# Kernel optimization log

Hardware: AMD Instinct MI355X
Metric: run time of the kernel (lower is better)

The kernel has to match this reference:

```python
import jax, jax.numpy as jnp
import numpy as np
from jax import lax

H = 128

def _lstm_gates(x, h, c, w_ih, w_hh, b_ih, b_hh):
    # PyTorch gate order: i, f, g, o
    g = x @ w_ih.T + h @ w_hh.T + b_ih + b_hh
    i, f, gg, o = jnp.split(g, 4, axis=-1)
    c_new = jax.nn.sigmoid(f) * c + jax.nn.sigmoid(i) * jnp.tanh(gg)
    h_new = jax.nn.sigmoid(o) * jnp.tanh(c_new)
    return h_new, c_new

def _lstm_layer(x_btF, w_ih, w_hh, b_ih, b_hh):
    B = x_btF.shape[0]
    h0 = jnp.zeros((B, H), x_btF.dtype)
    c0 = jnp.zeros((B, H), x_btF.dtype)
    def step(carry, xt):
        h, c = carry
        h, c = _lstm_gates(xt, h, c, w_ih, w_hh, b_ih, b_hh)
        return (h, c), h
    (h_T, c_T), ys = lax.scan(step, (h0, c0), jnp.swapaxes(x_btF, 0, 1))
    return jnp.swapaxes(ys, 0, 1), h_T, c_T

def setup_inputs() -> dict:
    key = jax.random.key(0)
    ks = jax.random.split(key, 20)
    B, T, D, P = 4096, 200, 2, 3
    s = 1.0 / np.sqrt(H)
    u = lambda k, shp: jax.random.uniform(k, shp, jnp.float32, -s, s)
    return {
        'x_hist': jax.random.normal(ks[0], (B, T, D), jnp.float32),
        'params': jax.random.normal(ks[1], (B, P), jnp.float32),
        'pred_len': 200,
        'w_ih0': u(ks[2], (4 * H, D)), 'w_hh0': u(ks[3], (4 * H, H)),
        'b_ih0': u(ks[4], (4 * H,)), 'b_hh0': u(ks[5], (4 * H,)),
        'w_ih1': u(ks[6], (4 * H, H)), 'w_hh1': u(ks[7], (4 * H, H)),
        'b_ih1': u(ks[8], (4 * H,)), 'b_hh1': u(ks[9], (4 * H,)),
        'dec_w_ih': u(ks[10], (4 * H, D + P)), 'dec_w_hh': u(ks[11], (4 * H, H)),
        'dec_b_ih': u(ks[12], (4 * H,)), 'dec_b_hh': u(ks[13], (4 * H,)),
        'proj_w': u(ks[14], (H, P)), 'proj_b': u(ks[15], (H,)),
        'out_w': u(ks[16], (2, H)), 'out_b': u(ks[17], (2,)),
    }

def reference(x_hist, params, pred_len, w_ih0, w_hh0, b_ih0, b_hh0,
              w_ih1, w_hh1, b_ih1, b_hh1, dec_w_ih, dec_w_hh, dec_b_ih,
              dec_b_hh, proj_w, proj_b, out_w, out_b):
    # 2-layer encoder LSTM; only last layer's final (h, c) are used
    y1, _, _ = _lstm_layer(x_hist, w_ih0, w_hh0, b_ih0, b_hh0)
    _, h_n, c_n = _lstm_layer(y1, w_ih1, w_hh1, b_ih1, b_hh1)
    h = h_n + params @ proj_w.T + proj_b
    c = c_n
    cur = x_hist[:, -1, :]
    def step(carry, _):
        h, c, cur = carry
        inp = jnp.concatenate([cur, params], axis=-1)
        h, c = _lstm_gates(inp, h, c, dec_w_ih, dec_w_hh, dec_b_ih, dec_b_hh)
        cur = h @ out_w.T + out_b
        return (h, c, cur), cur
    _, preds = lax.scan(step, (h, c, cur), None, length=pred_len)
    return jnp.swapaxes(preds, 0, 1)  # [B, pred_len, 2]
```

## Files before the change

kernel.cpp:

```cpp
#include <hip/hip_runtime.h>
#include <stdint.h>

typedef __bf16 bf16x8 __attribute__((ext_vector_type(8)));
typedef float  f32x4  __attribute__((ext_vector_type(4)));

#define PRED   200
#define TSTEPS 200
#define NBLK   256
#define ASTR   280
#define ALO    136
#define ABUFB  (16*ASTR*2)
#define W_BYTES 131072
#define A_OFF   W_BYTES
#define LDS_A   (A_OFF + 2*ABUFB)
#define STG_OFF (A_OFF + 2*ABUFB)
#define LDS_C   (STG_OFF + ABUFB)
#define CP_OFF  (A_OFF + 2*ABUFB)
#define CUR_OFF (CP_OFF + 1024)
#define LDS_D   (CUR_OFF + 128)

#define STATE_FLOATS ((size_t)NBLK*4*2048)

__device__ __forceinline__ float sigm(float x){ return 1.0f/(1.0f+__expf(-x)); }
__device__ __forceinline__ float tanhx(float x){
  float t=__expf(-2.0f*fabsf(x)); float y=(1.0f-t)/(1.0f+t); return copysignf(y,x);
}
__device__ __forceinline__ bf16x8 hi8(float4 a, float4 b){
  bf16x8 r; r[0]=(__bf16)a.x; r[1]=(__bf16)a.y; r[2]=(__bf16)a.z; r[3]=(__bf16)a.w;
  r[4]=(__bf16)b.x; r[5]=(__bf16)b.y; r[6]=(__bf16)b.z; r[7]=(__bf16)b.w; return r;
}
__device__ __forceinline__ bf16x8 lo8(float4 a, float4 b, bf16x8 h){
  bf16x8 r;
  r[0]=(__bf16)(a.x-(float)h[0]); r[1]=(__bf16)(a.y-(float)h[1]);
  r[2]=(__bf16)(a.z-(float)h[2]); r[3]=(__bf16)(a.w-(float)h[3]);
  r[4]=(__bf16)(b.x-(float)h[4]); r[5]=(__bf16)(b.y-(float)h[5]);
  r[6]=(__bf16)(b.z-(float)h[6]); r[7]=(__bf16)(b.w-(float)h[7]); return r;
}
#define MFMA(A,B,C) __builtin_amdgcn_mfma_f32_16x16x32_bf16((A),(B),(C),0,0,0)

__global__ void __launch_bounds__(512,2)
k_l0(const float* __restrict__ xh, const float* __restrict__ wih0,
     const float* __restrict__ whh0, const float* __restrict__ bih0,
     const float* __restrict__ bhh0, float* __restrict__ wsf,
     int chunkStart, int chunkLen, unsigned long long stageFloats)
{
  extern __shared__ char smem[];
  const int tid=threadIdx.x, wv=tid>>6, l=tid&63, c=l&15, qd=l>>4;
  const int hc=wv*16+c, blk=blockIdx.x, r0=blk*16;
  float* stf = wsf + stageFloats;
  #pragma unroll
  for (int i=0;i<16;++i){
    int f=i*8+wv, ntg=f>>2, kt=f&3;
    int g=(ntg&3)*128+(ntg>>2)*16+c, k=kt*32+qd*8;
    const float* s=whh0+g*128+k;
    *(bf16x8*)(smem+f*1024+l*16)=hi8(*(const float4*)s,*(const float4*)(s+4));
  }
  bf16x8 wlo[16];
  #pragma unroll
  for (int tt=0;tt<4;++tt)
    #pragma unroll
    for (int kt=0;kt<4;++kt){
      const float* s=whh0+(size_t)(tt*128+hc)*128+kt*32+qd*8;
      float4 a=*(const float4*)s, b=*(const float4*)(s+4);
      wlo[tt*4+kt]=lo8(a,b,hi8(a,b));
    }
  float b0[4], w0x[4], w0y[4];
  #pragma unroll
  for (int tt=0;tt<4;++tt){
    int g=tt*128+hc;
    b0[tt]=bih0[g]+bhh0[g]; w0x[tt]=wih0[2*g]; w0y[tt]=wih0[2*g+1];
  }
  float c0[4];
  {
    __bf16* B1=(__bf16*)(smem+A_OFF+ABUFB);
    const float* hst=stf+(size_t)(blk*4+0)*2048;
    const float* cst=stf+(size_t)(blk*4+1)*2048;
    #pragma unroll
    for (int i=0;i<4;++i){
      int e=tid*4+i, row=e>>7, col=e&127;
      float v=0.f; if(chunkStart) v=hst[e];
      __bf16 h=(__bf16)v;
      B1[row*ASTR+col]=h; B1[row*ASTR+ALO+col]=(__bf16)(v-(float)h);
    }
    #pragma unroll
    for (int j=0;j<4;++j){ float v=0.f; if(chunkStart) v=cst[(qd*4+j)*128+hc]; c0[j]=v; }
  }
  __syncthreads();
  for (int t=0;t<chunkLen;++t){
    const int p=t&1, tg=chunkStart+t;
    float2 xv[4];
    #pragma unroll
    for (int j=0;j<4;++j) xv[j]=*(const float2*)(xh+(size_t)(r0+qd*4+j)*400+tg*2);
    f32x4 acc[4];
    #pragma unroll
    for (int tt=0;tt<4;++tt) acc[tt]=(f32x4){b0[tt],b0[tt],b0[tt],b0[tt]};
    const char* Ar=smem+A_OFF+(size_t)(1-p)*ABUFB;
    #pragma unroll
    for (int kt=0;kt<4;++kt){
      bf16x8 ah=*(const bf16x8*)(Ar+(c*ASTR+kt*32+qd*8)*2);
      bf16x8 al=*(const bf16x8*)(Ar+(c*ASTR+ALO+kt*32+qd*8)*2);
      #pragma unroll
      for (int tt=0;tt<4;++tt){
        bf16x8 bh=*(const bf16x8*)(smem+(size_t)((wv*4+tt)*4+kt)*1024+l*16);
        acc[tt]=MFMA(ah,bh,acc[tt]);
        acc[tt]=MFMA(al,bh,acc[tt]);
        acc[tt]=MFMA(ah,wlo[tt*4+kt],acc[tt]);
      }
    }
    __bf16* Aw=(__bf16*)(smem+A_OFF+(size_t)p*ABUFB);
    float* h0o=wsf+((size_t)t*NBLK+blk)*2048;
    #pragma unroll
    for (int j=0;j<4;++j){
      float gi=acc[0][j]+xv[j].x*w0x[0]+xv[j].y*w0y[0];
      float gf=acc[1][j]+xv[j].x*w0x[1]+xv[j].y*w0y[1];
      float gg=acc[2][j]+xv[j].x*w0x[2]+xv[j].y*w0y[2];
      float go=acc[3][j]+xv[j].x*w0x[3]+xv[j].y*w0y[3];
      float cn=sigm(gf)*c0[j]+sigm(gi)*tanhx(gg); c0[j]=cn;
      float hn=sigm(go)*tanhx(cn);
      int row=qd*4+j;
      __bf16 hh=(__bf16)hn;
      Aw[row*ASTR+hc]=hh; Aw[row*ASTR+ALO+hc]=(__bf16)(hn-(float)hh);
      h0o[row*128+hc]=hn;
      if (t==chunkLen-1){
        stf[(size_t)(blk*4+0)*2048+row*128+hc]=hn;
        stf[(size_t)(blk*4+1)*2048+row*128+hc]=cn;
      }
    }
    __syncthreads();
  }
}

__global__ void __launch_bounds__(512,2)
k_l1(const float* __restrict__ wih1, const float* __restrict__ whh1,
     const float* __restrict__ bih1, const float* __restrict__ bhh1,
     float* __restrict__ wsf, int chunkStart, int chunkLen,
     unsigned long long stageFloats)
{
  extern __shared__ char smem[];
  const int tid=threadIdx.x, wv=tid>>6, l=tid&63, c=l&15, qd=l>>4;
  const int hc=wv*16+c, blk=blockIdx.x;
  float* stf = wsf + stageFloats;
  #pragma unroll
  for (int i=0;i<16;++i){
    int f=i*8+wv, ntg=f>>2, kt=f&3;
    int g=(ntg&3)*128+(ntg>>2)*16+c, k=kt*32+qd*8;
    const float* s=wih1+g*128+k;
    *(bf16x8*)(smem+f*1024+l*16)=hi8(*(const float4*)s,*(const float4*)(s+4));
  }
  bf16x8 whh[16], whl[16];
  #pragma unroll
  for (int tt=0;tt<4;++tt)
    #pragma unroll
    for (int kt=0;kt<4;++kt){
      const float* s2=whh1+(size_t)(tt*128+hc)*128+kt*32+qd*8;
      float4 a2=*(const float4*)s2, b2=*(const float4*)(s2+4);
      bf16x8 h2=hi8(a2,b2);
      whh[tt*4+kt]=h2; whl[tt*4+kt]=lo8(a2,b2,h2);
    }
  float b1v[4];
  #pragma unroll
  for (int tt=0;tt<4;++tt){ int g=tt*128+hc; b1v[tt]=bih1[g]+bhh1[g]; }
  float c1[4];
  {
    __bf16* B1=(__bf16*)(smem+A_OFF+ABUFB);
    const float* hst=stf+(size_t)(blk*4+2)*2048;
    const float* cst=stf+(size_t)(blk*4+3)*2048;
    #pragma unroll
    for (int i=0;i<4;++i){
      int e=tid*4+i, row=e>>7, col=e&127;
      float v=0.f; if(chunkStart) v=hst[e];
      __bf16 h=(__bf16)v;
      B1[row*ASTR+col]=h; B1[row*ASTR+ALO+col]=(__bf16)(v-(float)h);
    }
    #pragma unroll
    for (int j=0;j<4;++j){ float v=0.f; if(chunkStart) v=cst[(qd*4+j)*128+hc]; c1[j]=v; }
  }
  float4 r4=*(const float4*)(wsf+((size_t)0*NBLK+blk)*2048+tid*4);
  __syncthreads();
  for (int t=0;t<chunkLen;++t){
    const int p=t&1;
    {
      __bf16* ST=(__bf16*)(smem+STG_OFF);
      int e=tid*4, row=e>>7, col=e&127;
      #pragma unroll
      for (int i=0;i<4;++i){
        float v=r4[i]; __bf16 h=(__bf16)v;
        ST[row*ASTR+col+i]=h; ST[row*ASTR+ALO+col+i]=(__bf16)(v-(float)h);
      }
    }
    if (t+1<chunkLen) r4=*(const float4*)(wsf+((size_t)(t+1)*NBLK+blk)*2048+tid*4);
    __syncthreads();
    f32x4 acc[4];
    #pragma unroll
    for (int tt=0;tt<4;++tt) acc[tt]=(f32x4){b1v[tt],b1v[tt],b1v[tt],b1v[tt]};
    const char* Ar=smem+A_OFF+(size_t)(1-p)*ABUFB;
    const char* Sr=smem+STG_OFF;
    #pragma unroll
    for (int kt=0;kt<4;++kt){
      bf16x8 a0h=*(const bf16x8*)(Sr+(c*ASTR+kt*32+qd*8)*2);
      bf16x8 a0l=*(const bf16x8*)(Sr+(c*ASTR+ALO+kt*32+qd*8)*2);
      bf16x8 a1h=*(const bf16x8*)(Ar+(c*ASTR+kt*32+qd*8)*2);
      bf16x8 a1l=*(const bf16x8*)(Ar+(c*ASTR+ALO+kt*32+qd*8)*2);
      #pragma unroll
      for (int tt=0;tt<4;++tt){
        bf16x8 bh=*(const bf16x8*)(smem+(size_t)((wv*4+tt)*4+kt)*1024+l*16);
        const float* sw=wih1+(size_t)(tt*128+hc)*128+kt*32+qd*8;
        float4 wa=*(const float4*)sw, wb=*(const float4*)(sw+4);
        bf16x8 wl=lo8(wa,wb,hi8(wa,wb));
        acc[tt]=MFMA(a0h,bh,acc[tt]);
        acc[tt]=MFMA(a0l,bh,acc[tt]);
        acc[tt]=MFMA(a0h,wl,acc[tt]);
        acc[tt]=MFMA(a1h,whh[tt*4+kt],acc[tt]);
        acc[tt]=MFMA(a1l,whh[tt*4+kt],acc[tt]);
        acc[tt]=MFMA(a1h,whl[tt*4+kt],acc[tt]);
      }
    }
    __bf16* Aw=(__bf16*)(smem+A_OFF+(size_t)p*ABUFB);
    #pragma unroll
    for (int j=0;j<4;++j){
      float cn=sigm(acc[1][j])*c1[j]+sigm(acc[0][j])*tanhx(acc[2][j]); c1[j]=cn;
      float hn=sigm(acc[3][j])*tanhx(cn);
      int row=qd*4+j;
      __bf16 hh=(__bf16)hn;
      Aw[row*ASTR+hc]=hh; Aw[row*ASTR+ALO+hc]=(__bf16)(hn-(float)hh);
      if (t==chunkLen-1){
        stf[(size_t)(blk*4+2)*2048+row*128+hc]=hn;
        stf[(size_t)(blk*4+3)*2048+row*128+hc]=cn;
      }
    }
    __syncthreads();
  }
}

__global__ void __launch_bounds__(512,2)
k_dec(const float* __restrict__ xh, const float* __restrict__ pprm,
      const float* __restrict__ dwihp, const float* __restrict__ dwhh,
      const float* __restrict__ dbih, const float* __restrict__ dbhh,
      const float* __restrict__ pw, const float* __restrict__ pb,
      const float* __restrict__ ow, const float* __restrict__ ob,
      const float* __restrict__ wsf, float* __restrict__ out,
      unsigned long long stageFloats)
{
  extern __shared__ char smem[];
  const int tid=threadIdx.x, wv=tid>>6, l=tid&63, c=l&15, qd=l>>4;
  const int hc=wv*16+c, blk=blockIdx.x, r0=blk*16;
  const float* stf = wsf + stageFloats;
  #pragma unroll
  for (int i=0;i<16;++i){
    int f=i*8+wv, ntg=f>>2, kt=f&3;
    int g=(ntg&3)*128+(ntg>>2)*16+c, k=kt*32+qd*8;
    const float* s=dwhh+g*128+k;
    *(bf16x8*)(smem+f*1024+l*16)=hi8(*(const float4*)s,*(const float4*)(s+4));
  }
  bf16x8 wlo[16];
  #pragma unroll
  for (int tt=0;tt<4;++tt)
    #pragma unroll
    for (int kt=0;kt<4;++kt){
      const float* s=dwhh+(size_t)(tt*128+hc)*128+kt*32+qd*8;
      float4 a=*(const float4*)s, b=*(const float4*)(s+4);
      wlo[tt*4+kt]=lo8(a,b,hi8(a,b));
    }
  float dwi[4][5], db[4];
  #pragma unroll
  for (int tt=0;tt<4;++tt){
    int g=tt*128+hc;
    db[tt]=dbih[g]+dbhh[g];
    #pragma unroll
    for (int k=0;k<5;++k) dwi[tt][k]=dwihp[g*5+k];
  }
  float prj0=pw[hc*3+0], prj1=pw[hc*3+1], prj2=pw[hc*3+2], prjb=pb[hc];
  float ow0=ow[hc], ow1=ow[128+hc];
  float prm[4][3];
  #pragma unroll
  for (int j=0;j<4;++j){
    size_t r=(size_t)(r0+qd*4+j);
    prm[j][0]=pprm[r*3+0]; prm[j][1]=pprm[r*3+1]; prm[j][2]=pprm[r*3+2];
  }
  const float* h1s=stf+(size_t)(blk*4+2)*2048;
  const float* c1s=stf+(size_t)(blk*4+3)*2048;
  float c1[4];
  {
    __bf16* B0=(__bf16*)(smem+A_OFF);
    #pragma unroll
    for (int j=0;j<4;++j){
      int row=qd*4+j;
      float hd=h1s[row*128+hc]+prm[j][0]*prj0+prm[j][1]*prj1+prm[j][2]*prj2+prjb;
      __bf16 h=(__bf16)hd;
      B0[row*ASTR+hc]=h; B0[row*ASTR+ALO+hc]=(__bf16)(hd-(float)h);
      c1[j]=c1s[row*128+hc];
    }
  }
  float obv=0.f;
  if (tid<32){
    int r=tid>>1, d=tid&1;
    ((float*)(smem+CUR_OFF))[tid]=xh[(size_t)(r0+r)*400+199*2+d];
    obv=ob[d];
  }
  __syncthreads();
  for (int s=0;s<PRED;++s){
    const int q=s&1;
    float cur0[4], cur1[4];
    #pragma unroll
    for (int j=0;j<4;++j){
      cur0[j]=((const float*)(smem+CUR_OFF))[(qd*4+j)*2+0];
      cur1[j]=((const float*)(smem+CUR_OFF))[(qd*4+j)*2+1];
    }
    f32x4 acc[4];
    #pragma unroll
    for (int tt=0;tt<4;++tt) acc[tt]=(f32x4){db[tt],db[tt],db[tt],db[tt]};
    const char* Ar=smem+A_OFF+(size_t)q*ABUFB;
    #pragma unroll
    for (int kt=0;kt<4;++kt){
      bf16x8 ah=*(const bf16x8*)(Ar+(c*ASTR+kt*32+qd*8)*2);
      bf16x8 al=*(const bf16x8*)(Ar+(c*ASTR+ALO+kt*32+qd*8)*2);
      #pragma unroll
      for (int tt=0;tt<4;++tt){
        bf16x8 bh=*(const bf16x8*)(smem+(size_t)((wv*4+tt)*4+kt)*1024+l*16);
        acc[tt]=MFMA(ah,bh,acc[tt]);
        acc[tt]=MFMA(al,bh,acc[tt]);
        acc[tt]=MFMA(ah,wlo[tt*4+kt],acc[tt]);
      }
    }
    __bf16* Aw=(__bf16*)(smem+A_OFF+(size_t)(1-q)*ABUFB);
    float pc0[4], pc1[4];
    #pragma unroll
    for (int j=0;j<4;++j){
      float gi=acc[0][j]+cur0[j]*dwi[0][0]+cur1[j]*dwi[0][1]+prm[j][0]*dwi[0][2]+prm[j][1]*dwi[0][3]+prm[j][2]*dwi[0][4];
      float gf=acc[1][j]+cur0[j]*dwi[1][0]+cur1[j]*dwi[1][1]+prm[j][0]*dwi[1][2]+prm[j][1]*dwi[1][3]+prm[j][2]*dwi[1][4];
      float gg=acc[2][j]+cur0[j]*dwi[2][0]+cur1[j]*dwi[2][1]+prm[j][0]*dwi[2][2]+prm[j][1]*dwi[2][3]+prm[j][2]*dwi[2][4];
      float go=acc[3][j]+cur0[j]*dwi[3][0]+cur1[j]*dwi[3][1]+prm[j][0]*dwi[3][2]+prm[j][1]*dwi[3][3]+prm[j][2]*dwi[3][4];
      float cn=sigm(gf)*c1[j]+sigm(gi)*tanhx(gg); c1[j]=cn;
      float hn=sigm(go)*tanhx(cn);
      int row=qd*4+j;
      __bf16 hh=(__bf16)hn;
      Aw[row*ASTR+hc]=hh; Aw[row*ASTR+ALO+hc]=(__bf16)(hn-(float)hh);
      pc0[j]=hn*ow0; pc1[j]=hn*ow1;
    }
    #pragma unroll
    for (int m=1;m<16;m<<=1){
      #pragma unroll
      for (int j=0;j<4;++j){
        pc0[j]+=__shfl_xor(pc0[j],m,64);
        pc1[j]+=__shfl_xor(pc1[j],m,64);
      }
    }
    float* cp=(float*)(smem+CP_OFF);
    if (c==0){
      #pragma unroll
      for (int j=0;j<4;++j){
        cp[(wv*16+qd*4+j)*2+0]=pc0[j];
        cp[(wv*16+qd*4+j)*2+1]=pc1[j];
      }
    }
    __syncthreads();
    if (tid<32){
      int r=tid>>1, d=tid&1;
      float sv=obv;
      #pragma unroll
      for (int w2=0;w2<8;++w2) sv+=cp[(w2*16+r)*2+d];
      ((float*)(smem+CUR_OFF))[tid]=sv;
      out[(size_t)(r0+r)*400+s*2+d]=sv;
    }
    __syncthreads();
  }
}

extern "C" void kernel_launch(void* const* d_in, const int* in_sizes, int n_in,
                              void* d_out, int out_size, void* d_ws, size_t ws_size,
                              hipStream_t stream)
{
  (void)out_size;
  const int base = (n_in >= 19 && in_sizes[2] == 1) ? 3 : 2;
  const float* xh   = (const float*)d_in[0];
  const float* prm  = (const float*)d_in[1];
  const float* wih0 = (const float*)d_in[base+0];
  const float* whh0 = (const float*)d_in[base+1];
  const float* bih0 = (const float*)d_in[base+2];
  const float* bhh0 = (const float*)d_in[base+3];
  const float* wih1 = (const float*)d_in[base+4];
  const float* whh1 = (const float*)d_in[base+5];
  const float* bih1 = (const float*)d_in[base+6];
  const float* bhh1 = (const float*)d_in[base+7];
  const float* dwih = (const float*)d_in[base+8];
  const float* dwhh = (const float*)d_in[base+9];
  const float* dbih = (const float*)d_in[base+10];
  const float* dbhh = (const float*)d_in[base+11];
  const float* pw   = (const float*)d_in[base+12];
  const float* pb   = (const float*)d_in[base+13];
  const float* ow   = (const float*)d_in[base+14];
  const float* ob   = (const float*)d_in[base+15];
  float* wsf = (float*)d_ws;

  size_t wsFloats = ws_size / 4;
  size_t avail = (wsFloats > STATE_FLOATS) ? (wsFloats - STATE_FLOATS) : 0;
  int chunkLen = (int)(avail / ((size_t)NBLK * 2048));
  if (chunkLen > 50) chunkLen = 50;
  if (chunkLen < 1)  chunkLen = 1;
  unsigned long long stageFloats = (unsigned long long)chunkLen * NBLK * 2048;

  hipFuncSetAttribute((const void*)k_l0,  hipFuncAttributeMaxDynamicSharedMemorySize, LDS_A);
  hipFuncSetAttribute((const void*)k_l1,  hipFuncAttributeMaxDynamicSharedMemorySize, LDS_C);
  hipFuncSetAttribute((const void*)k_dec, hipFuncAttributeMaxDynamicSharedMemorySize, LDS_D);

  for (int k0 = 0; k0 < TSTEPS; k0 += chunkLen){
    int len = chunkLen; if (k0 + len > TSTEPS) len = TSTEPS - k0;
    k_l0<<<NBLK,512,LDS_A,stream>>>(xh, wih0, whh0, bih0, bhh0, wsf, k0, len, stageFloats);
    k_l1<<<NBLK,512,LDS_C,stream>>>(wih1, whh1, bih1, bhh1, wsf, k0, len, stageFloats);
  }
  k_dec<<<NBLK,512,LDS_D,stream>>>(xh, prm, dwih, dwhh, dbih, dbhh,
                                   pw, pb, ow, ob, wsf, (float*)d_out, stageFloats);
}
```

Before: 1.956 ms.

## Fold decoder output projection into recurrent weights and drop per-step reduction

The decoder now folds the output projection algebraically into the recurrent weights (W_hh + W_ih[:, :2] @ out_w) and the constant inputs (params, out_b) into a per-row bias, so the feedback input no longer has to be computed before the next gate matmul. The per-step cross-wave shuffle and LDS reduction and the second barrier go away; the output is computed off the critical path by wave 0 with a small MFMA. It also keeps the full hi and lo weights in registers with launch bounds of 1, uses a swizzled, conflict-free LDS layout, and splits the accumulators into two chains for more MFMA ILP. Folding the weights changes rounding slightly, adds a first-step correction term, and raises register pressure.

```diff
diff --git a/kernel.cpp b/kernel.cpp
--- a/kernel.cpp
+++ b/kernel.cpp
@@ -7,17 +7,18 @@
 #define PRED   200
 #define TSTEPS 200
 #define NBLK   256
+
 #define ASTR   280
 #define ALO    136
-#define ABUFB  (16*ASTR*2)
+#define ABUFE  (16*ASTR*2)
 #define W_BYTES 131072
 #define A_OFF   W_BYTES
-#define LDS_A   (A_OFF + 2*ABUFB)
-#define STG_OFF (A_OFF + 2*ABUFB)
-#define LDS_C   (STG_OFF + ABUFB)
-#define CP_OFF  (A_OFF + 2*ABUFB)
-#define CUR_OFF (CP_OFF + 1024)
-#define LDS_D   (CUR_OFF + 128)
+#define LDS_A   (A_OFF + 2*ABUFE)
+#define STG_OFF (A_OFF + 2*ABUFE)
+#define LDS_C   (STG_OFF + ABUFE)
+
+#define ABUFD  8192
+#define LDS_D  (2*ABUFD)
 
 #define STATE_FLOATS ((size_t)NBLK*4*2048)
 
@@ -37,6 +38,13 @@
   r[6]=(__bf16)(b.z-(float)h[6]); r[7]=(__bf16)(b.w-(float)h[7]); return r;
 }
 #define MFMA(A,B,C) __builtin_amdgcn_mfma_f32_16x16x32_bf16((A),(B),(C),0,0,0)
+
+__device__ __forceinline__ int aoff(int row, int col){
+  return row*512 + ((((col>>3) ^ (row&7)) << 4) | ((col&7)<<1));
+}
+__device__ __forceinline__ int frdoff(int c, int qd, int kt, int plane){
+  return c*512 + (((((kt<<2)+qd) ^ (c&7)) | (plane<<4)) << 4);
+}
 
 __global__ void __launch_bounds__(512,2)
 k_l0(const float* __restrict__ xh, const float* __restrict__ wih0,
@@ -72,7 +80,7 @@
   }
   float c0[4];
   {
-    __bf16* B1=(__bf16*)(smem+A_OFF+ABUFB);
+    __bf16* B1=(__bf16*)(smem+A_OFF+ABUFE);
     const float* hst=stf+(size_t)(blk*4+0)*2048;
     const float* cst=stf+(size_t)(blk*4+1)*2048;
     #pragma unroll
@@ -94,7 +102,7 @@
     f32x4 acc[4];
     #pragma unroll
     for (int tt=0;tt<4;++tt) acc[tt]=(f32x4){b0[tt],b0[tt],b0[tt],b0[tt]};
-    const char* Ar=smem+A_OFF+(size_t)(1-p)*ABUFB;
+    const char* Ar=smem+A_OFF+(size_t)(1-p)*ABUFE;
     #pragma unroll
     for (int kt=0;kt<4;++kt){
       bf16x8 ah=*(const bf16x8*)(Ar+(c*ASTR+kt*32+qd*8)*2);
@@ -107,7 +115,7 @@
         acc[tt]=MFMA(ah,wlo[tt*4+kt],acc[tt]);
       }
     }
-    __bf16* Aw=(__bf16*)(smem+A_OFF+(size_t)p*ABUFB);
+    __bf16* Aw=(__bf16*)(smem+A_OFF+(size_t)p*ABUFE);
     float* h0o=wsf+((size_t)t*NBLK+blk)*2048;
     #pragma unroll
     for (int j=0;j<4;++j){
@@ -162,7 +170,7 @@
   for (int tt=0;tt<4;++tt){ int g=tt*128+hc; b1v[tt]=bih1[g]+bhh1[g]; }
   float c1[4];
   {
-    __bf16* B1=(__bf16*)(smem+A_OFF+ABUFB);
+    __bf16* B1=(__bf16*)(smem+A_OFF+ABUFE);
     const float* hst=stf+(size_t)(blk*4+2)*2048;
     const float* cst=stf+(size_t)(blk*4+3)*2048;
     #pragma unroll
@@ -184,7 +192,7 @@
       int e=tid*4, row=e>>7, col=e&127;
       #pragma unroll
       for (int i=0;i<4;++i){
-        float v=r4[i]; __bf16 h=(__bf16)v;
+        float v=((const float*)&r4)[i]; __bf16 h=(__bf16)v;
         ST[row*ASTR+col+i]=h; ST[row*ASTR+ALO+col+i]=(__bf16)(v-(float)h);
       }
     }
@@ -193,7 +201,7 @@
     f32x4 acc[4];
     #pragma unroll
     for (int tt=0;tt<4;++tt) acc[tt]=(f32x4){b1v[tt],b1v[tt],b1v[tt],b1v[tt]};
-    const char* Ar=smem+A_OFF+(size_t)(1-p)*ABUFB;
+    const char* Ar=smem+A_OFF+(size_t)(1-p)*ABUFE;
     const char* Sr=smem+STG_OFF;
     #pragma unroll
     for (int kt=0;kt<4;++kt){
@@ -215,7 +223,7 @@
         acc[tt]=MFMA(a1h,whl[tt*4+kt],acc[tt]);
       }
     }
-    __bf16* Aw=(__bf16*)(smem+A_OFF+(size_t)p*ABUFB);
+    __bf16* Aw=(__bf16*)(smem+A_OFF+(size_t)p*ABUFE);
     #pragma unroll
     for (int j=0;j<4;++j){
       float cn=sigm(acc[1][j])*c1[j]+sigm(acc[0][j])*tanhx(acc[2][j]); c1[j]=cn;
@@ -232,7 +240,7 @@
   }
 }
 
-__global__ void __launch_bounds__(512,2)
+__global__ void __launch_bounds__(512,1)
 k_dec(const float* __restrict__ xh, const float* __restrict__ pprm,
       const float* __restrict__ dwihp, const float* __restrict__ dwhh,
       const float* __restrict__ dbih, const float* __restrict__ dbhh,
@@ -245,124 +253,156 @@
   const int tid=threadIdx.x, wv=tid>>6, l=tid&63, c=l&15, qd=l>>4;
   const int hc=wv*16+c, blk=blockIdx.x, r0=blk*16;
   const float* stf = wsf + stageFloats;
-  #pragma unroll
-  for (int i=0;i<16;++i){
-    int f=i*8+wv, ntg=f>>2, kt=f&3;
-    int g=(ntg&3)*128+(ntg>>2)*16+c, k=kt*32+qd*8;
-    const float* s=dwhh+g*128+k;
-    *(bf16x8*)(smem+f*1024+l*16)=hi8(*(const float4*)s,*(const float4*)(s+4));
-  }
-  bf16x8 wlo[16];
-  #pragma unroll
-  for (int tt=0;tt<4;++tt)
-    #pragma unroll
-    for (int kt=0;kt<4;++kt){
-      const float* s=dwhh+(size_t)(tt*128+hc)*128+kt*32+qd*8;
-      float4 a=*(const float4*)s, b=*(const float4*)(s+4);
-      wlo[tt*4+kt]=lo8(a,b,hi8(a,b));
-    }
-  float dwi[4][5], db[4];
-  #pragma unroll
-  for (int tt=0;tt<4;++tt){
-    int g=tt*128+hc;
-    db[tt]=dbih[g]+dbhh[g];
-    #pragma unroll
-    for (int k=0;k<5;++k) dwi[tt][k]=dwihp[g*5+k];
-  }
-  float prj0=pw[hc*3+0], prj1=pw[hc*3+1], prj2=pw[hc*3+2], prjb=pb[hc];
-  float ow0=ow[hc], ow1=ow[128+hc];
+  float ob0=ob[0], ob1=ob[1];
   float prm[4][3];
   #pragma unroll
   for (int j=0;j<4;++j){
     size_t r=(size_t)(r0+qd*4+j);
     prm[j][0]=pprm[r*3+0]; prm[j][1]=pprm[r*3+1]; prm[j][2]=pprm[r*3+2];
   }
+  float ptF[4][4], dw0[4], dw1[4];
+  #pragma unroll
+  for (int tt=0;tt<4;++tt){
+    int g=tt*128+hc;
+    float db=dbih[g]+dbhh[g];
+    dw0[tt]=dwihp[g*5+0]; dw1[tt]=dwihp[g*5+1];
+    #pragma unroll
+    for (int j=0;j<4;++j)
+      ptF[tt][j]=db+prm[j][0]*dwihp[g*5+2]+prm[j][1]*dwihp[g*5+3]+prm[j][2]*dwihp[g*5+4]
+                 +dw0[tt]*ob0+dw1[tt]*ob1;
+  }
+  bf16x8 whi[16], wlo[16];
+  #pragma unroll
+  for (int tt=0;tt<4;++tt)
+    #pragma unroll
+    for (int kt=0;kt<4;++kt){
+      int g=tt*128+hc, k=kt*32+qd*8;
+      float4 a=*(const float4*)(dwhh+(size_t)g*128+k), b=*(const float4*)(dwhh+(size_t)g*128+k+4);
+      float4 o0a=*(const float4*)(ow+k),     o0b=*(const float4*)(ow+k+4);
+      float4 o1a=*(const float4*)(ow+128+k), o1b=*(const float4*)(ow+128+k+4);
+      a.x+=dw0[tt]*o0a.x+dw1[tt]*o1a.x; a.y+=dw0[tt]*o0a.y+dw1[tt]*o1a.y;
+      a.z+=dw0[tt]*o0a.z+dw1[tt]*o1a.z; a.w+=dw0[tt]*o0a.w+dw1[tt]*o1a.w;
+      b.x+=dw0[tt]*o0b.x+dw1[tt]*o1b.x; b.y+=dw0[tt]*o0b.y+dw1[tt]*o1b.y;
+      b.z+=dw0[tt]*o0b.z+dw1[tt]*o1b.z; b.w+=dw0[tt]*o0b.w+dw1[tt]*o1b.w;
+      whi[tt*4+kt]=hi8(a,b); wlo[tt*4+kt]=lo8(a,b,whi[tt*4+kt]);
+    }
+  bf16x8 owh[4], owl[4];
+  #pragma unroll
+  for (int kt=0;kt<4;++kt){
+    int cc=(c<2)?c:0;
+    const float* s=ow+cc*128+kt*32+qd*8;
+    float4 a=*(const float4*)s, b=*(const float4*)(s+4);
+    if (c>=2){ a=(float4){0,0,0,0}; b=(float4){0,0,0,0}; }
+    owh[kt]=hi8(a,b); owl[kt]=lo8(a,b,owh[kt]);
+  }
   const float* h1s=stf+(size_t)(blk*4+2)*2048;
   const float* c1s=stf+(size_t)(blk*4+3)*2048;
-  float c1[4];
+  float c1[4], cx0[4], cx1[4];
   {
-    __bf16* B0=(__bf16*)(smem+A_OFF);
+    float prj0=pw[hc*3+0], prj1=pw[hc*3+1], prj2=pw[hc*3+2], prjb=pb[hc];
+    char* B0=smem;
     #pragma unroll
     for (int j=0;j<4;++j){
       int row=qd*4+j;
       float hd=h1s[row*128+hc]+prm[j][0]*prj0+prm[j][1]*prj1+prm[j][2]*prj2+prjb;
       __bf16 h=(__bf16)hd;
-      B0[row*ASTR+hc]=h; B0[row*ASTR+ALO+hc]=(__bf16)(hd-(float)h);
+      *(__bf16*)(B0+aoff(row,hc))=h;
+      *(__bf16*)(B0+aoff(row,hc+128))=(__bf16)(hd-(float)h);
       c1[j]=c1s[row*128+hc];
-    }
-  }
-  float obv=0.f;
-  if (tid<32){
-    int r=tid>>1, d=tid&1;
-    ((float*)(smem+CUR_OFF))[tid]=xh[(size_t)(r0+r)*400+199*2+d];
-    obv=ob[d];
+      float2 xx=*(const float2*)(xh+(size_t)(r0+row)*400+398);
+      cx0[j]=xx.x; cx1[j]=xx.y;
+    }
   }
   __syncthreads();
+  float corr0[4], corr1[4];
+  {
+    const char* Ar=smem;
+    f32x4 pv={0.f,0.f,0.f,0.f};
+    #pragma unroll
+    for (int kt=0;kt<4;++kt){
+      bf16x8 ah=*(const bf16x8*)(Ar+frdoff(c,qd,kt,0));
+      bf16x8 al=*(const bf16x8*)(Ar+frdoff(c,qd,kt,1));
+      pv=MFMA(ah,owh[kt],pv); pv=MFMA(al,owh[kt],pv); pv=MFMA(ah,owl[kt],pv);
+    }
+    #pragma unroll
+    for (int j=0;j<4;++j){
+      float p0=__shfl(pv[j], (l&48),   64);
+      float p1=__shfl(pv[j], (l&48)|1, 64);
+      corr0[j]=cx0[j]-(p0+ob0);
+      corr1[j]=cx1[j]-(p1+ob1);
+    }
+  }
   for (int s=0;s<PRED;++s){
     const int q=s&1;
-    float cur0[4], cur1[4];
+    const char* Ar=smem+(size_t)q*ABUFD;
+    bf16x8 ah[4], al[4];
+    #pragma unroll
+    for (int kt=0;kt<4;++kt){
+      ah[kt]=*(const bf16x8*)(Ar+frdoff(c,qd,kt,0));
+      al[kt]=*(const bf16x8*)(Ar+frdoff(c,qd,kt,1));
+    }
+    f32x4 aA[4], aB[4];
+    #pragma unroll
+    for (int tt=0;tt<4;++tt){ aA[tt]=(f32x4){ptF[tt][0],ptF[tt][1],ptF[tt][2],ptF[tt][3]}; aB[tt]=(f32x4){0.f,0.f,0.f,0.f}; }
+    #pragma unroll
+    for (int kt=0;kt<4;++kt)
+      #pragma unroll
+      for (int tt=0;tt<4;++tt){
+        f32x4* tgt=(kt<2)?&aA[tt]:&aB[tt];
+        *tgt=MFMA(ah[kt],whi[tt*4+kt],*tgt);
+        *tgt=MFMA(al[kt],whi[tt*4+kt],*tgt);
+        *tgt=MFMA(ah[kt],wlo[tt*4+kt],*tgt);
+      }
+    f32x4 pv={0.f,0.f,0.f,0.f};
+    if (wv==0){
+      #pragma unroll
+      for (int kt=0;kt<4;++kt){
+        pv=MFMA(ah[kt],owh[kt],pv); pv=MFMA(al[kt],owh[kt],pv); pv=MFMA(ah[kt],owl[kt],pv);
+      }
+    }
+    char* Aw=smem+(size_t)(1-q)*ABUFD;
     #pragma unroll
     for (int j=0;j<4;++j){
-      cur0[j]=((const float*)(smem+CUR_OFF))[(qd*4+j)*2+0];
-      cur1[j]=((const float*)(smem+CUR_OFF))[(qd*4+j)*2+1];
-    }
-    f32x4 acc[4];
-    #pragma unroll
-    for (int tt=0;tt<4;++tt) acc[tt]=(f32x4){db[tt],db[tt],db[tt],db[tt]};
-    const char* Ar=smem+A_OFF+(size_t)q*ABUFB;
-    #pragma unroll
-    for (int kt=0;kt<4;++kt){
-      bf16x8 ah=*(const bf16x8*)(Ar+(c*ASTR+kt*32+qd*8)*2);
-      bf16x8 al=*(const bf16x8*)(Ar+(c*ASTR+ALO+kt*32+qd*8)*2);
-      #pragma unroll
-      for (int tt=0;tt<4;++tt){
-        bf16x8 bh=*(const bf16x8*)(smem+(size_t)((wv*4+tt)*4+kt)*1024+l*16);
-        acc[tt]=MFMA(ah,bh,acc[tt]);
-        acc[tt]=MFMA(al,bh,acc[tt]);
-        acc[tt]=MFMA(ah,wlo[tt*4+kt],acc[tt]);
-      }
-    }
-    __bf16* Aw=(__bf16*)(smem+A_OFF+(size_t)(1-q)*ABUFB);
-    float pc0[4], pc1[4];
-    #pragma unroll
-    for (int j=0;j<4;++j){
-      float gi=acc[0][j]+cur0[j]*dwi[0][0]+cur1[j]*dwi[0][1]+prm[j][0]*dwi[0][2]+prm[j][1]*dwi[0][3]+prm[j][2]*dwi[0][4];
-      float gf=acc[1][j]+cur0[j]*dwi[1][0]+cur1[j]*dwi[1][1]+prm[j][0]*dwi[1][2]+prm[j][1]*dwi[1][3]+prm[j][2]*dwi[1][4];
-      float gg=acc[2][j]+cur0[j]*dwi[2][0]+cur1[j]*dwi[2][1]+prm[j][0]*dwi[2][2]+prm[j][1]*dwi[2][3]+prm[j][2]*dwi[2][4];
-      float go=acc[3][j]+cur0[j]*dwi[3][0]+cur1[j]*dwi[3][1]+prm[j][0]*dwi[3][2]+prm[j][1]*dwi[3][3]+prm[j][2]*dwi[3][4];
+      float gi=aA[0][j]+aB[0][j];
+      float gf=aA[1][j]+aB[1][j];
+      float gg=aA[2][j]+aB[2][j];
+      float go=aA[3][j]+aB[3][j];
+      if (s==0){
+        gi+=corr0[j]*dw0[0]+corr1[j]*dw1[0];
+        gf+=corr0[j]*dw0[1]+corr1[j]*dw1[1];
+        gg+=corr0[j]*dw0[2]+corr1[j]*dw1[2];
+        go+=corr0[j]*dw0[3]+corr1[j]*dw1[3];
+      }
       float cn=sigm(gf)*c1[j]+sigm(gi)*tanhx(gg); c1[j]=cn;
       float hn=sigm(go)*tanhx(cn);
       int row=qd*4+j;
       __bf16 hh=(__bf16)hn;
-      Aw[row*ASTR+hc]=hh; Aw[row*ASTR+ALO+hc]=(__bf16)(hn-(float)hh);
-      pc0[j]=hn*ow0; pc1[j]=hn*ow1;
-    }
-    #pragma unroll
-    for (int m=1;m<16;m<<=1){
-      #pragma unroll
-      for (int j=0;j<4;++j){
-        pc0[j]+=__shfl_xor(pc0[j],m,64);
-        pc1[j]+=__shfl_xor(pc1[j],m,64);
-      }
-    }
-    float* cp=(float*)(smem+CP_OFF);
-    if (c==0){
-      #pragma unroll
-      for (int j=0;j<4;++j){
-        cp[(wv*16+qd*4+j)*2+0]=pc0[j];
-        cp[(wv*16+qd*4+j)*2+1]=pc1[j];
-      }
+      *(__bf16*)(Aw+aoff(row,hc))=hh;
+      *(__bf16*)(Aw+aoff(row,hc+128))=(__bf16)(hn-(float)hh);
+    }
+    if (s && wv==0 && c<2){
+      float obv=c?ob1:ob0;
+      #pragma unroll
+      for (int j=0;j<4;++j)
+        out[(size_t)(r0+qd*4+j)*400+(s-1)*2+c]=pv[j]+obv;
     }
     __syncthreads();
-    if (tid<32){
-      int r=tid>>1, d=tid&1;
-      float sv=obv;
-      #pragma unroll
-      for (int w2=0;w2<8;++w2) sv+=cp[(w2*16+r)*2+d];
-      ((float*)(smem+CUR_OFF))[tid]=sv;
-      out[(size_t)(r0+r)*400+s*2+d]=sv;
-    }
-    __syncthreads();
+  }
+  if (wv==0){
+    const char* Ar=smem+(size_t)(PRED&1)*ABUFD;
+    f32x4 pv={0.f,0.f,0.f,0.f};
+    #pragma unroll
+    for (int kt=0;kt<4;++kt){
+      bf16x8 ah=*(const bf16x8*)(Ar+frdoff(c,qd,kt,0));
+      bf16x8 al=*(const bf16x8*)(Ar+frdoff(c,qd,kt,1));
+      pv=MFMA(ah,owh[kt],pv); pv=MFMA(al,owh[kt],pv); pv=MFMA(ah,owl[kt],pv);
+    }
+    if (c<2){
+      float obv=c?ob1:ob0;
+      #pragma unroll
+      for (int j=0;j<4;++j)
+        out[(size_t)(r0+qd*4+j)*400+(PRED-1)*2+c]=pv[j]+obv;
+    }
   }
 }
 
@@ -399,9 +439,8 @@
   if (chunkLen < 1)  chunkLen = 1;
   unsigned long long stageFloats = (unsigned long long)chunkLen * NBLK * 2048;
 
-  hipFuncSetAttribute((const void*)k_l0,  hipFuncAttributeMaxDynamicSharedMemorySize, LDS_A);
-  hipFuncSetAttribute((const void*)k_l1,  hipFuncAttributeMaxDynamicSharedMemorySize, LDS_C);
-  hipFuncSetAttribute((const void*)k_dec, hipFuncAttributeMaxDynamicSharedMemorySize, LDS_D);
+  hipFuncSetAttribute((const void*)k_l0, hipFuncAttributeMaxDynamicSharedMemorySize, LDS_A);
+  hipFuncSetAttribute((const void*)k_l1, hipFuncAttributeMaxDynamicSharedMemorySize, LDS_C);
 
   for (int k0 = 0; k0 < TSTEPS; k0 += chunkLen){
     int len = chunkLen; if (k0 + len > TSTEPS) len = TSTEPS - k0;
```

New measurement: 1.816 ms (median of 2 runs). -7.2%, faster.
